# Optimization experiments

Measured on AMD Instinct MI355X. Metric: run time of the kernel, lower is better.

Reference implementation:

```python
import jax, jax.numpy as jnp
import numpy as np

TOP_K = 8
NUM_EXPERTS = 32
CAPACITY = 1024


def setup_inputs() -> dict:
    key = jax.random.key(0)
    k1, k2, k3, k4 = jax.random.split(key, 4)
    B, S, H, E, F = 2, 1024, 1024, NUM_EXPERTS, 768
    return {
        "hidden_states": jax.random.normal(k1, (B, S, H), dtype=jnp.float32),
        "gate_weight": jax.random.normal(k2, (E, H), dtype=jnp.float32) * 0.02,
        "gate_up_proj": jax.random.normal(k3, (E, 2 * F, H), dtype=jnp.float32) * 0.02,
        "down_proj": jax.random.normal(k4, (E, H, F), dtype=jnp.float32) * 0.02,
    }


def reference(hidden_states, gate_weight, gate_up_proj, down_proj):
    B, S, H = hidden_states.shape
    E = gate_weight.shape[0]
    N = B * S
    x = hidden_states.reshape(N, H)

    # Router: fp32 softmax, top-k, renormalize (norm_topk_prob=True)
    logits = x @ gate_weight.T                                   # [N, E]
    probs = jax.nn.softmax(logits.astype(jnp.float32), axis=-1)
    topw, topi = jax.lax.top_k(probs, TOP_K)                     # [N, K]
    topw = topw / topw.sum(-1, keepdims=True)
    topw = topw.astype(x.dtype)

    # Flatten token-slot view (matches repeat_interleave ordering)
    flat_e = topi.reshape(-1)                                    # [N*K] int
    flat_w = topw.reshape(-1)                                    # [N*K]
    flat_x = jnp.repeat(x, TOP_K, axis=0)                        # [N*K, H]

    # Position of each slot within its expert (stable order, like stable argsort)
    oh = jax.nn.one_hot(flat_e, E, dtype=jnp.int32)              # [N*K, E]
    pos = (jnp.cumsum(oh, axis=0) * oh).sum(-1) - 1              # [N*K]

    # Dispatch into per-expert buffers [E, C, H]; grouped GEMMs; gather back
    buf = jnp.zeros((E, CAPACITY, H), x.dtype).at[flat_e, pos].set(flat_x, mode="drop")
    gu = jnp.einsum("ech,efh->ecf", buf, gate_up_proj)           # [E, C, 2F]
    gate, up = jnp.split(gu, 2, axis=-1)
    h = jax.nn.silu(gate) * up                                   # [E, C, F]
    eo = jnp.einsum("ecf,ehf->ech", h, down_proj)                # [E, C, H]
    tok_out = eo.at[flat_e, pos].get(mode="fill", fill_value=0)  # [N*K, H]

    out = (tok_out * flat_w[:, None]).reshape(N, TOP_K, H).sum(1)
    return out.reshape(B, S, H)
```

## Files before the change

kernel.cpp:

```cpp
#include <hip/hip_runtime.h>
#include <hip/hip_bf16.h>
#include <stdint.h>
#include <math.h>

#define NTOK  2048
#define HDIM  1024
#define FDIM  768
#define NEXP  32
#define TOPK  8
#define CAP   1024

typedef __attribute__((ext_vector_type(8))) short short8;
typedef __attribute__((ext_vector_type(4))) float f32x4;

__device__ __forceinline__ short f2bf(float f) {
  union { float f; uint32_t u; } c; c.f = f;
  uint32_t u = c.u;
  u += 0x7fffu + ((u >> 16) & 1u);
  return (short)(u >> 16);
}

__device__ __forceinline__ short8 pack8(float4 a, float4 b) {
  short8 r;
  r[0] = f2bf(a.x); r[1] = f2bf(a.y); r[2] = f2bf(a.z); r[3] = f2bf(a.w);
  r[4] = f2bf(b.x); r[5] = f2bf(b.y); r[6] = f2bf(b.z); r[7] = f2bf(b.w);
  return r;
}

__global__ __launch_bounds__(256) void router_kern(
    const float* __restrict__ x, const float* __restrict__ gw,
    int* __restrict__ cnt, int* __restrict__ slot_tok,
    float* __restrict__ slot_w, short* __restrict__ xb) {
  const int n0 = blockIdx.x * 8;
  const int t  = threadIdx.x;
  __shared__ float ls[8][32];

  const int e = t >> 3;
  const int j = t & 7;
  float acc[8];
#pragma unroll
  for (int i = 0; i < 8; ++i) acc[i] = 0.f;
  const float* gwe = gw + (size_t)e * HDIM;
  for (int i = 0; i < 128; ++i) {
    const int k = j + 8 * i;
    const float gv = gwe[k];
#pragma unroll
    for (int tok = 0; tok < 8; ++tok)
      acc[tok] += gv * x[(size_t)(n0 + tok) * HDIM + k];
  }
#pragma unroll
  for (int tok = 0; tok < 8; ++tok) {
    float v = acc[tok];
    v += __shfl_xor(v, 1); v += __shfl_xor(v, 2); v += __shfl_xor(v, 4);
    if (j == 0) ls[tok][e] = v;
  }
  __syncthreads();

  if (t < 8) {
    const int n = n0 + t;
    float lv[32];
#pragma unroll
    for (int i = 0; i < 32; ++i) lv[i] = ls[t][i];
    int   idx[TOPK];
    float val[TOPK];
    for (int kk = 0; kk < TOPK; ++kk) {
      float best = -INFINITY; int bi = 0;
      for (int i = 0; i < 32; ++i)
        if (lv[i] > best) { best = lv[i]; bi = i; }
      val[kk] = best; idx[kk] = bi; lv[bi] = -INFINITY;
    }
    const float m = val[0];
    float w[TOPK]; float wsum = 0.f;
    for (int kk = 0; kk < TOPK; ++kk) { w[kk] = __expf(val[kk] - m); wsum += w[kk]; }
    const float inv = 1.f / wsum;
    for (int kk = 0; kk < TOPK; ++kk) {
      const int ee = idx[kk];
      const int pos = atomicAdd(&cnt[ee], 1);
      if (pos < CAP) {
        slot_tok[ee * CAP + pos] = n * TOPK + kk;
        slot_w[ee * CAP + pos]   = w[kk] * inv;
      }
    }
  }

  const size_t base = (size_t)n0 * HDIM;
  for (int i = t; i < 8 * HDIM; i += 256)
    xb[base + i] = f2bf(x[base + i]);
}

__global__ __launch_bounds__(256) void gemm1_kern(
    const short* __restrict__ xb, const float* __restrict__ gup,
    const int* __restrict__ cnt, const int* __restrict__ slot_tok,
    short* __restrict__ hbuf) {
  const int e = blockIdx.z;
  const int mcnt = min(cnt[e], CAP);
  const int r0 = blockIdx.y * 64;
  if (r0 >= mcnt) return;
  const int f0 = blockIdx.x * 64;

  __shared__ short As[64 * 32];
  __shared__ short Bs[128 * 32];

  const int t = threadIdx.x;
  const int ar = t >> 2;
  const int koff = (t & 3) * 8;

  const short* aptr = nullptr;
  const bool avalid = (r0 + ar) < mcnt;
  if (avalid) {
    const int n = slot_tok[e * CAP + r0 + ar] >> 3;
    aptr = xb + (size_t)n * HDIM + koff;
  }
  const float* gp  = gup + ((size_t)e * (2 * FDIM) + (f0 + ar)) * HDIM + koff;
  const float* upp = gup + ((size_t)e * (2 * FDIM) + (FDIM + f0 + ar)) * HDIM + koff;

  const int wave = t >> 6, lane = t & 63;
  const int wm = (wave & 1) * 32, wf = (wave >> 1) * 32;
  const int lrow = lane & 15, lk = (lane >> 4) * 8;

  f32x4 accg[2][2], accu[2][2];
#pragma unroll
  for (int a = 0; a < 2; ++a)
#pragma unroll
    for (int b = 0; b < 2; ++b) {
      accg[a][b] = (f32x4){0.f, 0.f, 0.f, 0.f};
      accu[a][b] = (f32x4){0.f, 0.f, 0.f, 0.f};
    }

  for (int kb = 0; kb < HDIM; kb += 32) {
    if (avalid) *(uint4*)&As[ar * 32 + koff] = *(const uint4*)(aptr + kb);
    else        *(uint4*)&As[ar * 32 + koff] = make_uint4(0, 0, 0, 0);
    const float4 g0 = *(const float4*)(gp + kb);
    const float4 g1 = *(const float4*)(gp + kb + 4);
    const float4 u0 = *(const float4*)(upp + kb);
    const float4 u1 = *(const float4*)(upp + kb + 4);
    *(short8*)&Bs[ar * 32 + koff]        = pack8(g0, g1);
    *(short8*)&Bs[(64 + ar) * 32 + koff] = pack8(u0, u1);
    __syncthreads();

    short8 af[2], bg[2], bu[2];
    af[0] = *(const short8*)&As[(wm + lrow) * 32 + lk];
    af[1] = *(const short8*)&As[(wm + 16 + lrow) * 32 + lk];
    bg[0] = *(const short8*)&Bs[(wf + lrow) * 32 + lk];
    bg[1] = *(const short8*)&Bs[(wf + 16 + lrow) * 32 + lk];
    bu[0] = *(const short8*)&Bs[(64 + wf + lrow) * 32 + lk];
    bu[1] = *(const short8*)&Bs[(64 + wf + 16 + lrow) * 32 + lk];
#pragma unroll
    for (int mt = 0; mt < 2; ++mt)
#pragma unroll
      for (int nt = 0; nt < 2; ++nt) {
        accg[mt][nt] = __builtin_amdgcn_mfma_f32_16x16x32_bf16(af[mt], bg[nt], accg[mt][nt], 0, 0, 0);
        accu[mt][nt] = __builtin_amdgcn_mfma_f32_16x16x32_bf16(af[mt], bu[nt], accu[mt][nt], 0, 0, 0);
      }
    __syncthreads();
  }

#pragma unroll
  for (int mt = 0; mt < 2; ++mt)
#pragma unroll
    for (int nt = 0; nt < 2; ++nt)
#pragma unroll
      for (int r = 0; r < 4; ++r) {
        const int pos = r0 + wm + mt * 16 + (lane >> 4) * 4 + r;
        if (pos < mcnt) {
          const int f = f0 + wf + nt * 16 + (lane & 15);
          const float g = accg[mt][nt][r];
          const float u = accu[mt][nt][r];
          const float hv = (g / (1.f + __expf(-g))) * u;
          hbuf[((size_t)e * CAP + pos) * FDIM + f] = f2bf(hv);
        }
      }
}

__global__ __launch_bounds__(256) void gemm2_kern(
    const short* __restrict__ hbuf, const float* __restrict__ dwn,
    const int* __restrict__ cnt, const int* __restrict__ slot_tok,
    const float* __restrict__ slot_w, float* __restrict__ slot_out) {
  const int e = blockIdx.z;
  const int mcnt = min(cnt[e], CAP);
  const int r0 = blockIdx.y * 64;
  if (r0 >= mcnt) return;
  const int n0 = blockIdx.x * 64;

  __shared__ short As[64 * 32];
  __shared__ short Bs[64 * 32];

  const int t = threadIdx.x;
  const int ar = t >> 2;
  const int koff = (t & 3) * 8;

  const short* aptr = hbuf + ((size_t)e * CAP + (r0 + ar)) * FDIM + koff;
  const float* bp   = dwn + ((size_t)e * HDIM + (n0 + ar)) * FDIM + koff;

  const int wave = t >> 6, lane = t & 63;
  const int wm = (wave & 1) * 32, wn = (wave >> 1) * 32;
  const int lrow = lane & 15, lk = (lane >> 4) * 8;

  f32x4 acc[2][2];
#pragma unroll
  for (int a = 0; a < 2; ++a)
#pragma unroll
    for (int b = 0; b < 2; ++b) acc[a][b] = (f32x4){0.f, 0.f, 0.f, 0.f};

  for (int kb = 0; kb < FDIM; kb += 32) {
    *(uint4*)&As[ar * 32 + koff] = *(const uint4*)(aptr + kb);
    const float4 b0 = *(const float4*)(bp + kb);
    const float4 b1 = *(const float4*)(bp + kb + 4);
    *(short8*)&Bs[ar * 32 + koff] = pack8(b0, b1);
    __syncthreads();

    short8 af[2], bf[2];
    af[0] = *(const short8*)&As[(wm + lrow) * 32 + lk];
    af[1] = *(const short8*)&As[(wm + 16 + lrow) * 32 + lk];
    bf[0] = *(const short8*)&Bs[(wn + lrow) * 32 + lk];
    bf[1] = *(const short8*)&Bs[(wn + 16 + lrow) * 32 + lk];
#pragma unroll
    for (int mt = 0; mt < 2; ++mt)
#pragma unroll
      for (int nt = 0; nt < 2; ++nt)
        acc[mt][nt] = __builtin_amdgcn_mfma_f32_16x16x32_bf16(af[mt], bf[nt], acc[mt][nt], 0, 0, 0);
    __syncthreads();
  }

#pragma unroll
  for (int mt = 0; mt < 2; ++mt)
#pragma unroll
    for (int nt = 0; nt < 2; ++nt)
#pragma unroll
      for (int r = 0; r < 4; ++r) {
        const int pos = r0 + wm + mt * 16 + (lane >> 4) * 4 + r;
        if (pos < mcnt) {
          const int s = slot_tok[e * CAP + pos];
          const float w = slot_w[e * CAP + pos];
          const int col = n0 + wn + nt * 16 + (lane & 15);
          slot_out[(size_t)s * HDIM + col] = w * acc[mt][nt][r];
        }
      }
}

__global__ __launch_bounds__(256) void gather_kern(
    const float* __restrict__ so, float* __restrict__ out) {
  const int n = blockIdx.x;
  const int c = threadIdx.x * 4;
  float4 a = make_float4(0.f, 0.f, 0.f, 0.f);
#pragma unroll
  for (int k = 0; k < TOPK; ++k) {
    const float4 v = *(const float4*)&so[((size_t)(n * TOPK + k)) * HDIM + c];
    a.x += v.x; a.y += v.y; a.z += v.z; a.w += v.w;
  }
  *(float4*)&out[(size_t)n * HDIM + c] = a;
}

extern "C" void kernel_launch(void* const* d_in, const int* in_sizes, int n_in,
                              void* d_out, int out_size, void* d_ws, size_t ws_size,
                              hipStream_t stream) {
  const float* x   = (const float*)d_in[0];
  const float* gw  = (const float*)d_in[1];
  const float* gup = (const float*)d_in[2];
  const float* dwn = (const float*)d_in[3];
  float* out = (float*)d_out;

  char* ws = (char*)d_ws;
  int*   cnt      = (int*)(ws + 0);
  int*   slot_tok = (int*)(ws + 1024);
  float* slot_w   = (float*)(ws + 1024 + 131072);
  short* xb       = (short*)(ws + 524288);
  short* hbuf     = (short*)(ws + 524288 + 4194304);
  float* slot_out = (float*)(ws + 524288 + 4194304 + 50331648);

  hipMemsetAsync(cnt, 0, 1024, stream);
  router_kern<<<NTOK / 8, 256, 0, stream>>>(x, gw, cnt, slot_tok, slot_w, xb);
  gemm1_kern<<<dim3(FDIM / 64, CAP / 64, NEXP), 256, 0, stream>>>(xb, gup, cnt, slot_tok, hbuf);
  gemm2_kern<<<dim3(HDIM / 64, CAP / 64, NEXP), 256, 0, stream>>>(hbuf, dwn, cnt, slot_tok, slot_w, slot_out);
  gather_kern<<<NTOK, 256, 0, stream>>>(slot_out, out);
}
```

Measured before the change: 618.9 us.

## Pre-convert weights to bf16, use direct-to-LDS loads, larger tiles, atomic combine

Adds separate kernels that convert the gate/up and down weights to bf16 into a workspace buffer. The GEMMs can then load bf16 directly into LDS with global_load_lds instead of converting fp32 in-loop, which removes redundant weight conversion and halves weight read bytes per tile. The GEMM tiles grow to 128 rows, and gemm1 is split into two F-halves so the converted buffer fits. The slot_out buffer and gather kernel are replaced by atomicAdd into a zeroed output, at the cost of extra conversion passes, atomic contention, and non-deterministic summation order.

```diff
diff --git a/kernel.cpp b/kernel.cpp
--- a/kernel.cpp
+++ b/kernel.cpp
@@ -1,5 +1,4 @@
 #include <hip/hip_runtime.h>
-#include <hip/hip_bf16.h>
 #include <stdint.h>
 #include <math.h>
 
@@ -25,6 +24,41 @@
   r[0] = f2bf(a.x); r[1] = f2bf(a.y); r[2] = f2bf(a.z); r[3] = f2bf(a.w);
   r[4] = f2bf(b.x); r[5] = f2bf(b.y); r[6] = f2bf(b.z); r[7] = f2bf(b.w);
   return r;
+}
+
+__device__ __forceinline__ void gload16(const short* g, short* l) {
+  __builtin_amdgcn_global_load_lds(
+      (__attribute__((address_space(1))) uint32_t*)g,
+      (__attribute__((address_space(3))) uint32_t*)l, 16, 0, 0);
+}
+
+__global__ __launch_bounds__(256) void cvt_gup_kern(
+    const float* __restrict__ gup, short* __restrict__ W, int f_off) {
+  const size_t N8 = (size_t)NEXP * 768 * HDIM / 8;
+  const size_t stride = (size_t)gridDim.x * 256;
+  for (size_t i = (size_t)blockIdx.x * 256 + threadIdx.x; i < N8; i += stride) {
+    const int row = (int)(i >> 7);
+    const int k0  = (int)(i & 127) * 8;
+    const int e   = row / 768;
+    const int rg  = row - e * 768;
+    const int half = rg / 384;
+    const int fr   = rg - half * 384;
+    const size_t src = ((size_t)(e * 1536 + half * 768 + f_off + fr)) * HDIM + k0;
+    const float4 a = *(const float4*)(gup + src);
+    const float4 b = *(const float4*)(gup + src + 4);
+    *(short8*)(W + i * 8) = pack8(a, b);
+  }
+}
+
+__global__ __launch_bounds__(256) void cvt_dwn_kern(
+    const float* __restrict__ dwn, short* __restrict__ W) {
+  const size_t N8 = (size_t)NEXP * HDIM * FDIM / 8;
+  const size_t stride = (size_t)gridDim.x * 256;
+  for (size_t i = (size_t)blockIdx.x * 256 + threadIdx.x; i < N8; i += stride) {
+    const float4 a = *(const float4*)(dwn + i * 8);
+    const float4 b = *(const float4*)(dwn + i * 8 + 4);
+    *(short8*)(W + i * 8) = pack8(a, b);
+  }
 }
 
 __global__ __launch_bounds__(256) void router_kern(
@@ -89,38 +123,48 @@
 }
 
 __global__ __launch_bounds__(256) void gemm1_kern(
-    const short* __restrict__ xb, const float* __restrict__ gup,
+    const short* __restrict__ xb, const short* __restrict__ W,
     const int* __restrict__ cnt, const int* __restrict__ slot_tok,
-    short* __restrict__ hbuf) {
+    short* __restrict__ hbuf, int f_off) {
   const int e = blockIdx.z;
   const int mcnt = min(cnt[e], CAP);
-  const int r0 = blockIdx.y * 64;
+  const int r0 = blockIdx.y * 128;
   if (r0 >= mcnt) return;
   const int f0 = blockIdx.x * 64;
 
-  __shared__ short As[64 * 32];
-  __shared__ short Bs[128 * 32];
+  __shared__ short As[128 * 32];
+  __shared__ short Bg[64 * 32];
+  __shared__ short Bu[64 * 32];
 
   const int t = threadIdx.x;
-  const int ar = t >> 2;
-  const int koff = (t & 3) * 8;
-
-  const short* aptr = nullptr;
-  const bool avalid = (r0 + ar) < mcnt;
-  if (avalid) {
-    const int n = slot_tok[e * CAP + r0 + ar] >> 3;
-    aptr = xb + (size_t)n * HDIM + koff;
-  }
-  const float* gp  = gup + ((size_t)e * (2 * FDIM) + (f0 + ar)) * HDIM + koff;
-  const float* upp = gup + ((size_t)e * (2 * FDIM) + (FDIM + f0 + ar)) * HDIM + koff;
-
   const int wave = t >> 6, lane = t & 63;
-  const int wm = (wave & 1) * 32, wf = (wave >> 1) * 32;
+
+  const int la0 = wave * 128 + lane;
+  const int la1 = la0 + 64;
+  const int arow0 = la0 >> 2, aseg0 = la0 & 3;
+  const int arow1 = la1 >> 2, aseg1 = la1 & 3;
+  int tok0 = 0, tok1 = 0;
+  if (r0 + arow0 < mcnt) tok0 = slot_tok[e * CAP + r0 + arow0] >> 3;
+  if (r0 + arow1 < mcnt) tok1 = slot_tok[e * CAP + r0 + arow1] >> 3;
+  const short* aSrc0 = xb + (size_t)tok0 * HDIM + aseg0 * 8;
+  const short* aSrc1 = xb + (size_t)tok1 * HDIM + aseg1 * 8;
+  short* aDst0 = As + wave * 1024;
+  short* aDst1 = As + wave * 1024 + 512;
+
+  const int brow = t >> 2, bseg = t & 3;
+  const size_t gRow = (size_t)(e * 768 + f0 + brow);
+  const size_t uRow = gRow + 384;
+  const short* gSrc = W + gRow * HDIM + bseg * 8;
+  const short* uSrc = W + uRow * HDIM + bseg * 8;
+  short* gDst = Bg + wave * 512;
+  short* uDst = Bu + wave * 512;
+
+  const int wm = (wave & 1) * 64, wf = (wave >> 1) * 32;
   const int lrow = lane & 15, lk = (lane >> 4) * 8;
 
-  f32x4 accg[2][2], accu[2][2];
-#pragma unroll
-  for (int a = 0; a < 2; ++a)
+  f32x4 accg[4][2], accu[4][2];
+#pragma unroll
+  for (int a = 0; a < 4; ++a)
 #pragma unroll
     for (int b = 0; b < 2; ++b) {
       accg[a][b] = (f32x4){0.f, 0.f, 0.f, 0.f};
@@ -128,25 +172,23 @@
     }
 
   for (int kb = 0; kb < HDIM; kb += 32) {
-    if (avalid) *(uint4*)&As[ar * 32 + koff] = *(const uint4*)(aptr + kb);
-    else        *(uint4*)&As[ar * 32 + koff] = make_uint4(0, 0, 0, 0);
-    const float4 g0 = *(const float4*)(gp + kb);
-    const float4 g1 = *(const float4*)(gp + kb + 4);
-    const float4 u0 = *(const float4*)(upp + kb);
-    const float4 u1 = *(const float4*)(upp + kb + 4);
-    *(short8*)&Bs[ar * 32 + koff]        = pack8(g0, g1);
-    *(short8*)&Bs[(64 + ar) * 32 + koff] = pack8(u0, u1);
+    gload16(aSrc0 + kb, aDst0);
+    gload16(aSrc1 + kb, aDst1);
+    gload16(gSrc + kb, gDst);
+    gload16(uSrc + kb, uDst);
     __syncthreads();
 
-    short8 af[2], bg[2], bu[2];
-    af[0] = *(const short8*)&As[(wm + lrow) * 32 + lk];
-    af[1] = *(const short8*)&As[(wm + 16 + lrow) * 32 + lk];
-    bg[0] = *(const short8*)&Bs[(wf + lrow) * 32 + lk];
-    bg[1] = *(const short8*)&Bs[(wf + 16 + lrow) * 32 + lk];
-    bu[0] = *(const short8*)&Bs[(64 + wf + lrow) * 32 + lk];
-    bu[1] = *(const short8*)&Bs[(64 + wf + 16 + lrow) * 32 + lk];
-#pragma unroll
-    for (int mt = 0; mt < 2; ++mt)
+    short8 af[4], bg[2], bu[2];
+#pragma unroll
+    for (int mt = 0; mt < 4; ++mt)
+      af[mt] = *(const short8*)&As[(wm + mt * 16 + lrow) * 32 + lk];
+#pragma unroll
+    for (int nt = 0; nt < 2; ++nt) {
+      bg[nt] = *(const short8*)&Bg[(wf + nt * 16 + lrow) * 32 + lk];
+      bu[nt] = *(const short8*)&Bu[(wf + nt * 16 + lrow) * 32 + lk];
+    }
+#pragma unroll
+    for (int mt = 0; mt < 4; ++mt)
 #pragma unroll
       for (int nt = 0; nt < 2; ++nt) {
         accg[mt][nt] = __builtin_amdgcn_mfma_f32_16x16x32_bf16(af[mt], bg[nt], accg[mt][nt], 0, 0, 0);
@@ -156,99 +198,96 @@
   }
 
 #pragma unroll
-  for (int mt = 0; mt < 2; ++mt)
-#pragma unroll
-    for (int nt = 0; nt < 2; ++nt)
-#pragma unroll
-      for (int r = 0; r < 4; ++r) {
-        const int pos = r0 + wm + mt * 16 + (lane >> 4) * 4 + r;
-        if (pos < mcnt) {
-          const int f = f0 + wf + nt * 16 + (lane & 15);
-          const float g = accg[mt][nt][r];
-          const float u = accu[mt][nt][r];
+  for (int mt = 0; mt < 4; ++mt)
+#pragma unroll
+    for (int rr = 0; rr < 4; ++rr) {
+      const int pos = r0 + wm + mt * 16 + (lane >> 4) * 4 + rr;
+      if (pos < mcnt) {
+#pragma unroll
+        for (int nt = 0; nt < 2; ++nt) {
+          const float g = accg[mt][nt][rr];
+          const float u = accu[mt][nt][rr];
           const float hv = (g / (1.f + __expf(-g))) * u;
-          hbuf[((size_t)e * CAP + pos) * FDIM + f] = f2bf(hv);
+          hbuf[((size_t)e * CAP + pos) * FDIM + f_off + f0 + wf + nt * 16 + (lane & 15)] = f2bf(hv);
         }
       }
+    }
 }
 
 __global__ __launch_bounds__(256) void gemm2_kern(
-    const short* __restrict__ hbuf, const float* __restrict__ dwn,
+    const short* __restrict__ hbuf, const short* __restrict__ W,
     const int* __restrict__ cnt, const int* __restrict__ slot_tok,
-    const float* __restrict__ slot_w, float* __restrict__ slot_out) {
+    const float* __restrict__ slot_w, float* __restrict__ out) {
   const int e = blockIdx.z;
   const int mcnt = min(cnt[e], CAP);
-  const int r0 = blockIdx.y * 64;
+  const int r0 = blockIdx.y * 128;
   if (r0 >= mcnt) return;
-  const int n0 = blockIdx.x * 64;
-
-  __shared__ short As[64 * 32];
-  __shared__ short Bs[64 * 32];
+  const int n0 = blockIdx.x * 128;
+
+  __shared__ short As[128 * 32];
+  __shared__ short Bs[128 * 32];
 
   const int t = threadIdx.x;
-  const int ar = t >> 2;
-  const int koff = (t & 3) * 8;
-
-  const short* aptr = hbuf + ((size_t)e * CAP + (r0 + ar)) * FDIM + koff;
-  const float* bp   = dwn + ((size_t)e * HDIM + (n0 + ar)) * FDIM + koff;
-
   const int wave = t >> 6, lane = t & 63;
-  const int wm = (wave & 1) * 32, wn = (wave >> 1) * 32;
+
+  const int l0 = wave * 128 + lane;
+  const int l1 = l0 + 64;
+  const int ar0 = l0 >> 2, as0 = l0 & 3;
+  const int ar1 = l1 >> 2, as1 = l1 & 3;
+  const short* aSrc0 = hbuf + ((size_t)e * CAP + r0 + ar0) * FDIM + as0 * 8;
+  const short* aSrc1 = hbuf + ((size_t)e * CAP + r0 + ar1) * FDIM + as1 * 8;
+  const short* bSrc0 = W + ((size_t)e * HDIM + n0 + ar0) * FDIM + as0 * 8;
+  const short* bSrc1 = W + ((size_t)e * HDIM + n0 + ar1) * FDIM + as1 * 8;
+  short* aDst0 = As + wave * 1024;
+  short* aDst1 = As + wave * 1024 + 512;
+  short* bDst0 = Bs + wave * 1024;
+  short* bDst1 = Bs + wave * 1024 + 512;
+
+  const int wm = (wave & 1) * 64, wn = (wave >> 1) * 64;
   const int lrow = lane & 15, lk = (lane >> 4) * 8;
 
-  f32x4 acc[2][2];
-#pragma unroll
-  for (int a = 0; a < 2; ++a)
-#pragma unroll
-    for (int b = 0; b < 2; ++b) acc[a][b] = (f32x4){0.f, 0.f, 0.f, 0.f};
+  f32x4 acc[4][4];
+#pragma unroll
+  for (int a = 0; a < 4; ++a)
+#pragma unroll
+    for (int b = 0; b < 4; ++b) acc[a][b] = (f32x4){0.f, 0.f, 0.f, 0.f};
 
   for (int kb = 0; kb < FDIM; kb += 32) {
-    *(uint4*)&As[ar * 32 + koff] = *(const uint4*)(aptr + kb);
-    const float4 b0 = *(const float4*)(bp + kb);
-    const float4 b1 = *(const float4*)(bp + kb + 4);
-    *(short8*)&Bs[ar * 32 + koff] = pack8(b0, b1);
+    gload16(aSrc0 + kb, aDst0);
+    gload16(aSrc1 + kb, aDst1);
+    gload16(bSrc0 + kb, bDst0);
+    gload16(bSrc1 + kb, bDst1);
     __syncthreads();
 
-    short8 af[2], bf[2];
-    af[0] = *(const short8*)&As[(wm + lrow) * 32 + lk];
-    af[1] = *(const short8*)&As[(wm + 16 + lrow) * 32 + lk];
-    bf[0] = *(const short8*)&Bs[(wn + lrow) * 32 + lk];
-    bf[1] = *(const short8*)&Bs[(wn + 16 + lrow) * 32 + lk];
-#pragma unroll
-    for (int mt = 0; mt < 2; ++mt)
-#pragma unroll
-      for (int nt = 0; nt < 2; ++nt)
+    short8 af[4], bf[4];
+#pragma unroll
+    for (int i = 0; i < 4; ++i) {
+      af[i] = *(const short8*)&As[(wm + i * 16 + lrow) * 32 + lk];
+      bf[i] = *(const short8*)&Bs[(wn + i * 16 + lrow) * 32 + lk];
+    }
+#pragma unroll
+    for (int mt = 0; mt < 4; ++mt)
+#pragma unroll
+      for (int nt = 0; nt < 4; ++nt)
         acc[mt][nt] = __builtin_amdgcn_mfma_f32_16x16x32_bf16(af[mt], bf[nt], acc[mt][nt], 0, 0, 0);
     __syncthreads();
   }
 
 #pragma unroll
-  for (int mt = 0; mt < 2; ++mt)
-#pragma unroll
-    for (int nt = 0; nt < 2; ++nt)
-#pragma unroll
-      for (int r = 0; r < 4; ++r) {
-        const int pos = r0 + wm + mt * 16 + (lane >> 4) * 4 + r;
-        if (pos < mcnt) {
-          const int s = slot_tok[e * CAP + pos];
-          const float w = slot_w[e * CAP + pos];
-          const int col = n0 + wn + nt * 16 + (lane & 15);
-          slot_out[(size_t)s * HDIM + col] = w * acc[mt][nt][r];
-        }
+  for (int mt = 0; mt < 4; ++mt)
+#pragma unroll
+    for (int rr = 0; rr < 4; ++rr) {
+      const int pos = r0 + wm + mt * 16 + (lane >> 4) * 4 + rr;
+      if (pos < mcnt) {
+        const int s = slot_tok[e * CAP + pos];
+        const float w = slot_w[e * CAP + pos];
+        const int n = s >> 3;
+        float* orow = out + (size_t)n * HDIM + n0 + wn + (lane & 15);
+#pragma unroll
+        for (int nt = 0; nt < 4; ++nt)
+          atomicAdd(orow + nt * 16, w * acc[mt][nt][rr]);
       }
-}
-
-__global__ __launch_bounds__(256) void gather_kern(
-    const float* __restrict__ so, float* __restrict__ out) {
-  const int n = blockIdx.x;
-  const int c = threadIdx.x * 4;
-  float4 a = make_float4(0.f, 0.f, 0.f, 0.f);
-#pragma unroll
-  for (int k = 0; k < TOPK; ++k) {
-    const float4 v = *(const float4*)&so[((size_t)(n * TOPK + k)) * HDIM + c];
-    a.x += v.x; a.y += v.y; a.z += v.z; a.w += v.w;
-  }
-  *(float4*)&out[(size_t)n * HDIM + c] = a;
+    }
 }
 
 extern "C" void kernel_launch(void* const* d_in, const int* in_sizes, int n_in,
@@ -265,12 +304,18 @@
   int*   slot_tok = (int*)(ws + 1024);
   float* slot_w   = (float*)(ws + 1024 + 131072);
   short* xb       = (short*)(ws + 524288);
-  short* hbuf     = (short*)(ws + 524288 + 4194304);
-  float* slot_out = (float*)(ws + 524288 + 4194304 + 50331648);
+  short* hbuf     = (short*)(ws + 4718592);
+  short* W        = (short*)(ws + 55050240);
 
   hipMemsetAsync(cnt, 0, 1024, stream);
+  hipMemsetAsync(out, 0, (size_t)NTOK * HDIM * sizeof(float), stream);
+
   router_kern<<<NTOK / 8, 256, 0, stream>>>(x, gw, cnt, slot_tok, slot_w, xb);
-  gemm1_kern<<<dim3(FDIM / 64, CAP / 64, NEXP), 256, 0, stream>>>(xb, gup, cnt, slot_tok, hbuf);
-  gemm2_kern<<<dim3(HDIM / 64, CAP / 64, NEXP), 256, 0, stream>>>(hbuf, dwn, cnt, slot_tok, slot_w, slot_out);
-  gather_kern<<<NTOK, 256, 0, stream>>>(slot_out, out);
-}
+
+  cvt_gup_kern<<<2048, 256, 0, stream>>>(gup, W, 0);
+  gemm1_kern<<<dim3(384 / 64, CAP / 128, NEXP), 256, 0, stream>>>(xb, W, cnt, slot_tok, hbuf, 0);
+  cvt_gup_kern<<<2048, 256, 0, stream>>>(gup, W, 384);
+  gemm1_kern<<<dim3(384 / 64, CAP / 128, NEXP), 256, 0, stream>>>(xb, W, cnt, slot_tok, hbuf, 384);
+  cvt_dwn_kern<<<2048, 256, 0, stream>>>(dwn, W);
+  gemm2_kern<<<dim3(HDIM / 128, CAP / 128, NEXP), 256, 0, stream>>>(hbuf, W, cnt, slot_tok, slot_w, out);
+}
```

New measurement: 630.4 us. About the same (+1.8%).
